# Kernel tuning notes

Hardware: AMD Instinct MI355X
Metric: run time of the kernel (lower is better)

Reference implementation:

```python
import jax, jax.numpy as jnp
import numpy as np

N, E, H, G = 50000, 500000, 64, 64


def _ln(x, g, b):
    m = jnp.mean(x, -1, keepdims=True)
    v = jnp.var(x, -1, keepdims=True)
    return (x - m) * jax.lax.rsqrt(v + 1e-5) * g + b


def _mlp_ln(x, w1, b1, w2, b2, g, be):
    # Linear -> ReLU -> (Dropout eval no-op) -> Linear -> LayerNorm
    h = jax.nn.relu(x @ w1 + b1)
    return _ln(h @ w2 + b2, g, be)


def setup_inputs() -> dict:
    key = jax.random.key(0)
    ks = jax.random.split(key, 24)
    w = lambda i, s: jax.random.normal(ks[i], s, dtype=jnp.float32) * 0.1
    z = lambda s: jnp.zeros(s, jnp.float32)
    o = lambda s: jnp.ones(s, jnp.float32)
    inp = {
        'x': jax.random.normal(ks[0], (N, 3), dtype=jnp.float32),
        'edge_index': jax.random.randint(ks[1], (2, E), 0, N),
        'edge_attr': jax.random.normal(ks[2], (E, 3), dtype=jnp.float32),
        'batch': jnp.sort(jax.random.randint(ks[3], (N,), 0, G)),
        'ne_w1': w(4, (3, H)), 'ne_b1': z((H,)), 'ne_w2': w(5, (H, H)), 'ne_b2': z((H,)), 'ne_g': o((H,)), 'ne_be': z((H,)),
        'ee_w1': w(6, (3, H)), 'ee_b1': z((H,)), 'ee_w2': w(7, (H, H)), 'ee_b2': z((H,)), 'ee_g': o((H,)), 'ee_be': z((H,)),
        'gin0_eps': z((1,)), 'gin0_w1': w(8, (H, H)), 'gin0_b1': z((H,)), 'gin0_w2': w(9, (H, H)), 'gin0_b2': z((H,)), 'gin0_g': o((H,)), 'gin0_be': z((H,)),
        'gin1_eps': z((1,)), 'gin1_w1': w(10, (H, H)), 'gin1_b1': z((H,)), 'gin1_w2': w(11, (H, H)), 'gin1_b2': z((H,)), 'gin1_g': o((H,)), 'gin1_be': z((H,)),
        'gp_w': w(12, (H, H)), 'gp_b': z((H,)), 'gp_g': o((H,)), 'gp_be': z((H,)),
        'ep_w1': w(13, (4 * H, 2 * H)), 'ep_b1': z((2 * H,)),
        'ep_w2': w(14, (2 * H, H)), 'ep_b2': z((H,)),
        'ep_w3': w(15, (H, 1)), 'ep_b3': z((1,)),
    }
    return inp


def reference(x, edge_index, edge_attr, batch,
              ne_w1, ne_b1, ne_w2, ne_b2, ne_g, ne_be,
              ee_w1, ee_b1, ee_w2, ee_b2, ee_g, ee_be,
              gin0_eps, gin0_w1, gin0_b1, gin0_w2, gin0_b2, gin0_g, gin0_be,
              gin1_eps, gin1_w1, gin1_b1, gin1_w2, gin1_b2, gin1_g, gin1_be,
              gp_w, gp_b, gp_g, gp_be,
              ep_w1, ep_b1, ep_w2, ep_b2, ep_w3, ep_b3):
    src, dst = edge_index[0], edge_index[1]
    # encoders
    h = _mlp_ln(x, ne_w1, ne_b1, ne_w2, ne_b2, ne_g, ne_be)            # [N, H]
    ef = _mlp_ln(edge_attr, ee_w1, ee_b1, ee_w2, ee_b2, ee_g, ee_be)   # [E, H]
    # GINEConv layer 0: mlp((1+eps)*x + scatter_add(relu(x_src + e)))
    msg = jax.nn.relu(h[src] + ef)
    aggr = jnp.zeros_like(h).at[dst].add(msg)
    h = _mlp_ln((1.0 + gin0_eps) * h + aggr, gin0_w1, gin0_b1, gin0_w2, gin0_b2, gin0_g, gin0_be)
    h = jax.nn.relu(h)  # inter-layer activation (dropout eval no-op)
    # GINEConv layer 1
    msg = jax.nn.relu(h[src] + ef)
    aggr = jnp.zeros_like(h).at[dst].add(msg)
    h = _mlp_ln((1.0 + gin1_eps) * h + aggr, gin1_w1, gin1_b1, gin1_w2, gin1_b2, gin1_g, gin1_be)
    # global mean pool over graphs
    seg = jax.ops.segment_sum(h, batch, num_segments=G)                            # [G, H]
    cnt = jax.ops.segment_sum(jnp.ones((h.shape[0], 1), h.dtype), batch, num_segments=G)
    gp = seg / jnp.maximum(cnt, 1.0)
    gf = _ln(jax.nn.relu(gp @ gp_w + gp_b), gp_g, gp_be)                           # [G, H]
    # edge predictor on [src | dst | global | edge] = [E, 4H]
    c = jnp.concatenate([h[src], h[dst], gf[batch[src]], ef], axis=-1)
    t = jnp.tanh(c @ ep_w1 + ep_b1)
    t = jnp.tanh(t @ ep_w2 + ep_b2)
    return jax.nn.sigmoid(t @ ep_w3 + ep_b3)  # [E, 1]
```

## Files before the change

kernel.cpp:

```cpp
#include <hip/hip_runtime.h>
#include <hip/hip_bf16.h>

typedef unsigned int uint;
typedef unsigned short ushort;
typedef __attribute__((ext_vector_type(8))) short short8;
typedef __attribute__((ext_vector_type(4))) float floatx4;

__device__ __forceinline__ float bf2f(ushort u) { return __uint_as_float(((uint)u) << 16); }
__device__ __forceinline__ ushort f2bf(float f) {
  __bf16 h = (__bf16)f;
  ushort u;
  __builtin_memcpy(&u, &h, 2);
  return u;
}
__device__ __forceinline__ float ldf(const void* p, long i, int m) {
  if (m) return bf2f(((const ushort*)p)[i]);
  return ((const float*)p)[i];
}
__device__ __forceinline__ int get_md(const uint* mdp) {
  return (mdp[0] == 0x3F800000u) ? 0 : 1;
}
__device__ __forceinline__ float fast_rcp(float x) { return __builtin_amdgcn_rcpf(x); }
__device__ __forceinline__ float tanh_fast(float x) {
  float e = __builtin_amdgcn_exp2f(2.8853900818f * x);
  return fmaf(-2.f, fast_rcp(1.f + e), 1.f);
}
__device__ __forceinline__ float sigmoid_fast(float x) {
  float e = __builtin_amdgcn_exp2f(-1.4426950409f * x);
  return fast_rcp(1.f + e);
}
__device__ __forceinline__ void gll16(const void* g, void* l) {
  __builtin_amdgcn_global_load_lds(
      (const __attribute__((address_space(1))) uint*)g,
      (__attribute__((address_space(3))) uint*)l, 16, 0, 0);
}

__global__ __launch_bounds__(256) void k_enc_mfma(
    const void* __restrict__ in, int R,
    const void* __restrict__ w1, const void* __restrict__ b1,
    const ushort* __restrict__ w2sw_, const void* __restrict__ b2,
    const void* __restrict__ gam, const void* __restrict__ bet,
    ushort* __restrict__ outp, ushort* __restrict__ outp2,
    const int* __restrict__ epos, const uint* __restrict__ mdp)
{
  __shared__ float xs[64*3];
  __shared__ float w1s[192], b1s[64], b2s[64], gs[64], bs2[64];
  __shared__ __align__(16) ushort T_s[64 * 72];
  int md = get_md(mdp);
  int tid = threadIdx.x;
  long e0 = (long)blockIdx.x * 64;
  if (tid < 192) {
    w1s[tid] = ldf(w1, tid, md);
    int row = tid / 3, cc = tid - row*3;
    long e = e0 + row;
    xs[tid] = (e < R) ? ldf(in, e*3 + cc, md) : 0.f;
  }
  if (tid < 64) { b1s[tid] = ldf(b1, tid, md); b2s[tid] = ldf(b2, tid, md);
                  gs[tid] = ldf(gam, tid, md); bs2[tid] = ldf(bet, tid, md); }
  __syncthreads();
  int lane = tid & 63, wv = tid >> 6;
  int quad = lane >> 4, mm = lane & 15;
  float x0 = xs[(wv*16 + mm)*3 + 0];
  float x1 = xs[(wv*16 + mm)*3 + 1];
  float x2 = xs[(wv*16 + mm)*3 + 2];
  short8 af[2];
#pragma unroll
  for (int s = 0; s < 2; ++s) {
#pragma unroll
    for (int j = 0; j < 8; ++j) {
      int f = s*32 + quad*8 + j;
      float hv = fmaxf(b1s[f] + x0*w1s[f] + x1*w1s[64+f] + x2*w1s[128+f], 0.f);
      af[s][j] = (short)f2bf(hv);
    }
  }
  floatx4 acc[4] = {};
  const short8* Bp = (const short8*)w2sw_;
#pragma unroll
  for (int s = 0; s < 2; ++s) {
#pragma unroll
    for (int t = 0; t < 4; ++t) {
      short8 b = Bp[(s*4 + t)*64 + lane];
      acc[t] = __builtin_amdgcn_mfma_f32_16x16x32_bf16(af[s], b, acc[t], 0, 0, 0);
    }
  }
  float vv[4][4];
#pragma unroll
  for (int t = 0; t < 4; ++t) {
    float bb = b2s[mm + 16*t];
#pragma unroll
    for (int r = 0; r < 4; ++r) vv[t][r] = acc[t][r] + bb;
  }
  float mr[4], vr[4];
#pragma unroll
  for (int r = 0; r < 4; ++r) {
    float s = vv[0][r] + vv[1][r] + vv[2][r] + vv[3][r];
#pragma unroll
    for (int off = 1; off < 16; off <<= 1) s += __shfl_xor(s, off);
    mr[r] = s * 0.015625f;
    float q = 0.f;
#pragma unroll
    for (int t = 0; t < 4; ++t) { float d = vv[t][r] - mr[r]; q = fmaf(d, d, q); }
#pragma unroll
    for (int off = 1; off < 16; off <<= 1) q += __shfl_xor(q, off);
    vr[r] = rsqrtf(q * 0.015625f + 1e-5f);
  }
#pragma unroll
  for (int t = 0; t < 4; ++t) {
    int col = mm + 16*t;
    float g = gs[col], be = bs2[col];
#pragma unroll
    for (int r = 0; r < 4; ++r)
      T_s[(wv*16 + quad*4 + r)*72 + col] = f2bf((vv[t][r] - mr[r]) * vr[r] * g + be);
  }
  __syncthreads();
#pragma unroll
  for (int i = 0; i < 2; ++i) {
    int gi = tid + 256*i;
    int row = gi >> 3, c = gi & 7;
    long e = e0 + row;
    if (e < R) {
      uint4 v = *(const uint4*)&T_s[row*72 + c*8];
      if (outp)
        ((uint4*)(outp + e*64))[c] = v;
      if (outp2)
        ((uint4*)(outp2 + (long)epos[e]*64))[c] = v;
    }
  }
}

__global__ __launch_bounds__(256) void k_swz(
    const void* __restrict__ w1, const void* __restrict__ w2,
    const void* __restrict__ w2e, const void* __restrict__ w2n,
    const void* __restrict__ gw10, const void* __restrict__ gw20,
    const void* __restrict__ gw11, const void* __restrict__ gw21,
    ushort* __restrict__ w1sw, ushort* __restrict__ w2sw,
    ushort* __restrict__ ew2sw, ushort* __restrict__ nw2sw,
    ushort* __restrict__ g0w1sw, ushort* __restrict__ g0w2sw,
    ushort* __restrict__ g1w1sw, ushort* __restrict__ g1w2sw,
    int* __restrict__ deg, float* __restrict__ gsum, int Nn,
    const uint* __restrict__ mdp)
{
  int md = get_md(mdp);
  int i = blockIdx.x * 256 + threadIdx.x;
  int nthr = gridDim.x * 256;
  for (int k = i; k < Nn; k += nthr) deg[k] = 0;
  for (int k = i; k < 64*64 + 64; k += nthr) gsum[k] = 0.f;
  if (i < 32768) {
    int q = i & 7, lane = (i >> 3) & 63, tt = (i >> 9) & 7, s = i >> 12;
    int k = s*32 + (lane >> 4)*8 + q, n = (lane & 15) + 16*tt;
    w1sw[i] = f2bf(ldf(w1, k*128 + n, md));
  }
  if (i < 8192) {
    int q = i & 7, lane = (i >> 3) & 63, tt = (i >> 9) & 3, s = i >> 11;
    int k = s*32 + (lane >> 4)*8 + q, n = (lane & 15) + 16*tt;
    int src = k*64 + n;
    w2sw[i]   = f2bf(ldf(w2,   src, md));
    ew2sw[i]  = f2bf(ldf(w2e,  src, md));
    nw2sw[i]  = f2bf(ldf(w2n,  src, md));
    g0w1sw[i] = f2bf(ldf(gw10, src, md));
    g0w2sw[i] = f2bf(ldf(gw20, src, md));
    g1w1sw[i] = f2bf(ldf(gw11, src, md));
    g1w2sw[i] = f2bf(ldf(gw21, src, md));
  }
}

__global__ __launch_bounds__(256) void k_deg(
    const int* __restrict__ ei, int* __restrict__ deg, int E_)
{
  int e = blockIdx.x * 256 + threadIdx.x;
  if (e < E_) atomicAdd(&deg[ei[E_ + e]], 1);
}

__global__ __launch_bounds__(256) void k_scan1(
    const int* __restrict__ deg, int* __restrict__ rs, int* __restrict__ bsum, int Nn)
{
  __shared__ int ls[256];
  int tid = threadIdx.x;
  int i = blockIdx.x * 256 + tid;
  int v = (i < Nn) ? deg[i] : 0;
  ls[tid] = v;
  __syncthreads();
  for (int off = 1; off < 256; off <<= 1) {
    int t = (tid >= off) ? ls[tid - off] : 0;
    __syncthreads();
    ls[tid] += t;
    __syncthreads();
  }
  if (i < Nn) rs[i] = ls[tid] - v;
  if (tid == 255) bsum[blockIdx.x] = ls[255];
}

__global__ __launch_bounds__(256) void k_scan2(
    int* __restrict__ bsum, int nb, int* __restrict__ rs, int Nn)
{
  __shared__ int ls[256];
  int tid = threadIdx.x;
  int chunk = (nb + 255) / 256;
  int c0 = tid * chunk, c1 = min(c0 + chunk, nb);
  int sum = 0;
  for (int i = c0; i < c1; ++i) sum += bsum[i];
  ls[tid] = sum;
  __syncthreads();
  for (int off = 1; off < 256; off <<= 1) {
    int t = (tid >= off) ? ls[tid - off] : 0;
    __syncthreads();
    ls[tid] += t;
    __syncthreads();
  }
  int run = ls[tid] - sum;
  for (int i = c0; i < c1; ++i) { int d = bsum[i]; bsum[i] = run; run += d; }
  if (tid == 255) rs[Nn] = ls[255];
}

__global__ __launch_bounds__(256) void k_scan3(
    int* __restrict__ rs, int* __restrict__ cur,
    const int* __restrict__ bsum, int Nn)
{
  int i = blockIdx.x * 256 + threadIdx.x;
  if (i < Nn) {
    int v = rs[i] + bsum[blockIdx.x];
    rs[i] = v;
    cur[i] = v;
  }
}

__global__ __launch_bounds__(256) void k_fill(
    const int* __restrict__ ei, int* __restrict__ cur,
    int2* __restrict__ ep, int* __restrict__ epos, int E_)
{
  int e = blockIdx.x * 256 + threadIdx.x;
  if (e < E_) {
    int s = ei[e];
    int d = ei[E_ + e];
    int p = atomicAdd(&cur[d], 1);
    ep[p] = make_int2(e, s);
    epos[e] = p;
  }
}

__global__ __launch_bounds__(256) void k_aggr(
    const ushort* __restrict__ hbu, const ushort* __restrict__ efp,
    const int2* __restrict__ ep, const int* __restrict__ rs,
    float* __restrict__ aggr, int Nn)
{
  int gw = (blockIdx.x * 256 + threadIdx.x) >> 6;
  int j = threadIdx.x & 63;
  if (gw >= Nn) return;
  int s0 = rs[gw], s1 = rs[gw + 1];
  float acc = 0.f;
  int idx = s0;
  for (; idx + 2 <= s1; idx += 2) {
    int2 a = ep[idx];
    int2 b = ep[idx + 1];
    float fA = bf2f(efp[(long)idx*64 + j]);
    float fB = bf2f(efp[(long)(idx+1)*64 + j]);
    float hA = bf2f(hbu[(long)a.y*64 + j]);
    float hB = bf2f(hbu[(long)b.y*64 + j]);
    acc += fmaxf(hA + fA, 0.f) + fmaxf(hB + fB, 0.f);
  }
  if (idx < s1) {
    int2 a = ep[idx];
    acc += fmaxf(bf2f(hbu[(long)a.y*64 + j]) + bf2f(efp[(long)idx*64 + j]), 0.f);
  }
  aggr[(long)gw*64 + j] = acc;
}

__global__ __launch_bounds__(256) void k_gine_mfma(
    const ushort* __restrict__ hbin, const float* __restrict__ aggr, int Nn,
    const void* __restrict__ epsp,
    const ushort* __restrict__ w1sw_, const void* __restrict__ b1,
    const ushort* __restrict__ w2sw_, const void* __restrict__ b2,
    const void* __restrict__ gam, const void* __restrict__ bet,
    ushort* __restrict__ hbout, int post_relu, const uint* __restrict__ mdp)
{
  __shared__ __align__(16) ushort Ws1[4096], Ws2[4096];
  __shared__ __align__(16) ushort T_s[64 * 72];
  __shared__ float b1s[64], b2s[64], gs[64], bs2[64];
  int md = get_md(mdp);
  int tid = threadIdx.x;
  {
    const uint4* p1 = (const uint4*)w1sw_;
    const uint4* p2 = (const uint4*)w2sw_;
    ((uint4*)Ws1)[tid] = p1[tid];
    ((uint4*)Ws1)[tid + 256] = p1[tid + 256];
    ((uint4*)Ws2)[tid] = p2[tid];
    ((uint4*)Ws2)[tid + 256] = p2[tid + 256];
  }
  if (tid < 64) { b1s[tid] = ldf(b1, tid, md); b2s[tid] = ldf(b2, tid, md);
                  gs[tid] = ldf(gam, tid, md); bs2[tid] = ldf(bet, tid, md); }
  float ope = 1.f + ldf(epsp, 0, md);
  int lane = tid & 63, wv = tid >> 6;
  int quad = lane >> 4, mm = lane & 15;
  long node = (long)blockIdx.x * 64 + wv*16 + mm;
  long nc = (node < Nn) ? node : (long)(Nn - 1);
  const ushort* hrow = hbin + nc*64;
  const float*  arow = aggr + nc*64;
  short8 af[2];
#pragma unroll
  for (int s = 0; s < 2; ++s) {
    int c = s*4 + quad;
    short8 hv = *(const short8*)(hrow + c*8);
    float4 a0 = *(const float4*)(arow + c*8);
    float4 a1 = *(const float4*)(arow + c*8 + 4);
    float uu[8];
    uu[0] = fmaf(bf2f((ushort)hv[0]), ope, a0.x);
    uu[1] = fmaf(bf2f((ushort)hv[1]), ope, a0.y);
    uu[2] = fmaf(bf2f((ushort)hv[2]), ope, a0.z);
    uu[3] = fmaf(bf2f((ushort)hv[3]), ope, a0.w);
    uu[4] = fmaf(bf2f((ushort)hv[4]), ope, a1.x);
    uu[5] = fmaf(bf2f((ushort)hv[5]), ope, a1.y);
    uu[6] = fmaf(bf2f((ushort)hv[6]), ope, a1.z);
    uu[7] = fmaf(bf2f((ushort)hv[7]), ope, a1.w);
#pragma unroll
    for (int j = 0; j < 8; ++j) af[s][j] = (short)f2bf(uu[j]);
  }
  __syncthreads();
  floatx4 acc[4] = {};
#pragma unroll
  for (int s = 0; s < 2; ++s) {
#pragma unroll
    for (int t = 0; t < 4; ++t) {
      short8 b = *(const short8*)&Ws1[((s*4 + t)*64 + lane)*8];
      acc[t] = __builtin_amdgcn_mfma_f32_16x16x32_bf16(af[s], b, acc[t], 0, 0, 0);
    }
  }
#pragma unroll
  for (int t = 0; t < 4; ++t) {
    int col = mm + 16*t;
    float bb = b1s[col];
#pragma unroll
    for (int r = 0; r < 4; ++r)
      T_s[(wv*16 + quad*4 + r)*72 + col] = f2bf(fmaxf(acc[t][r] + bb, 0.f));
  }
  __syncthreads();
  short8 af2[2];
#pragma unroll
  for (int s = 0; s < 2; ++s)
    af2[s] = *(const short8*)&T_s[(wv*16 + mm)*72 + s*32 + quad*8];
  floatx4 acc2[4] = {};
#pragma unroll
  for (int s = 0; s < 2; ++s) {
#pragma unroll
    for (int t = 0; t < 4; ++t) {
      short8 b = *(const short8*)&Ws2[((s*4 + t)*64 + lane)*8];
      acc2[t] = __builtin_amdgcn_mfma_f32_16x16x32_bf16(af2[s], b, acc2[t], 0, 0, 0);
    }
  }
  float vv[4][4];
#pragma unroll
  for (int t = 0; t < 4; ++t) {
    float bb = b2s[mm + 16*t];
#pragma unroll
    for (int r = 0; r < 4; ++r) vv[t][r] = acc2[t][r] + bb;
  }
  float mr[4], vr[4];
#pragma unroll
  for (int r = 0; r < 4; ++r) {
    float s = vv[0][r] + vv[1][r] + vv[2][r] + vv[3][r];
#pragma unroll
    for (int off = 1; off < 16; off <<= 1) s += __shfl_xor(s, off);
    mr[r] = s * 0.015625f;
    float q = 0.f;
#pragma unroll
    for (int t = 0; t < 4; ++t) { float d = vv[t][r] - mr[r]; q = fmaf(d, d, q); }
#pragma unroll
    for (int off = 1; off < 16; off <<= 1) q += __shfl_xor(q, off);
    vr[r] = rsqrtf(q * 0.015625f + 1e-5f);
  }
  __syncthreads();
#pragma unroll
  for (int t = 0; t < 4; ++t) {
    int col = mm + 16*t;
    float g = gs[col], be = bs2[col];
#pragma unroll
    for (int r = 0; r < 4; ++r) {
      float o = (vv[t][r] - mr[r]) * vr[r] * g + be;
      if (post_relu) o = fmaxf(o, 0.f);
      T_s[(wv*16 + quad*4 + r)*72 + col] = f2bf(o);
    }
  }
  __syncthreads();
#pragma unroll
  for (int i = 0; i < 2; ++i) {
    int gi = tid + 256*i;
    int row = gi >> 3, c = gi & 7;
    long n2 = (long)blockIdx.x * 64 + row;
    if (n2 < Nn)
      ((uint4*)(hbout + n2*64))[c] = *(const uint4*)&T_s[row*72 + c*8];
  }
}

__global__ __launch_bounds__(256) void k_pool_f(
    const ushort* __restrict__ hbu, const int* __restrict__ batch,
    float* __restrict__ gsum, float* __restrict__ gcnt, int Nn)
{
  int gw = (blockIdx.x * 256 + threadIdx.x) >> 6;
  int j = threadIdx.x & 63;
  long r0 = (long)gw * 64;
  if (r0 >= Nn) return;
  long rend = min(r0 + 64, (long)Nn);
  float acc = 0.f; int cur = batch[r0]; int run = 0;
  for (long r = r0; r < rend; ++r) {
    int g = batch[r];
    if (g != cur) {
      atomicAdd(&gsum[cur*64 + j], acc);
      if (j == 0) atomicAdd(&gcnt[cur], (float)run);
      acc = 0.f; run = 0; cur = g;
    }
    acc += bf2f(hbu[r*64 + j]);
    run++;
  }
  atomicAdd(&gsum[cur*64 + j], acc);
  if (j == 0) atomicAdd(&gcnt[cur], (float)run);
}

__global__ __launch_bounds__(64) void k_pool_fin_f(
    const float* __restrict__ gsum, const float* __restrict__ gcnt,
    const void* __restrict__ gpw, const void* __restrict__ gpb,
    const void* __restrict__ gpg, const void* __restrict__ gpbe,
    ushort* __restrict__ gfb, const uint* __restrict__ mdp)
{
  __shared__ float wgs[4096];
  __shared__ float us[64];
  int md = get_md(mdp);
  int j = threadIdx.x;
  int g = blockIdx.x;
  for (int i = j; i < 4096; i += 64) wgs[i] = ldf(gpw, i, md);
  float ic = 1.f / fmaxf(gcnt[g], 1.f);
  us[j] = gsum[g*64 + j] * ic;
  __syncthreads();
  float t = ldf(gpb, j, md);
#pragma unroll
  for (int k = 0; k < 64; ++k) t = fmaf(us[k], wgs[k*64 + j], t);
  t = fmaxf(t, 0.f);
  float m = t;
#pragma unroll
  for (int off = 1; off < 64; off <<= 1) m += __shfl_xor(m, off);
  m *= 0.015625f;
  float d = t - m;
  float v = d * d;
#pragma unroll
  for (int off = 1; off < 64; off <<= 1) v += __shfl_xor(v, off);
  float rs = rsqrtf(v * 0.015625f + 1e-5f);
  gfb[g*64 + j] = f2bf(d * rs * ldf(gpg, j, md) + ldf(gpbe, j, md));
}

__global__ __launch_bounds__(1024, 4) void k_pred_mfma(
    const ushort* __restrict__ hb, const ushort* __restrict__ efp,
    const int* __restrict__ epos,
    const ushort* __restrict__ gfb, const int* __restrict__ ei,
    const int* __restrict__ batch,
    const ushort* __restrict__ w1sw, const ushort* __restrict__ w2sw,
    const void* __restrict__ pb1, const void* __restrict__ pb2,
    const void* __restrict__ pw3, const void* __restrict__ pb3,
    void* __restrict__ out, int E_, const uint* __restrict__ mdp)
{
  __shared__ __align__(16) ushort W1s[32768];
  __shared__ __align__(16) ushort W2s[8192];
  __shared__ __align__(16) ushort T_s[16 * 16*72];
  __shared__ float b1s[128], b2s[64], w3s[64];
  int md = get_md(mdp);
  int tid = threadIdx.x;
  {
    const uint4* w1p = (const uint4*)w1sw;
#pragma unroll
    for (int i = 0; i < 4; ++i)
      ((uint4*)W1s)[tid + 1024*i] = w1p[tid + 1024*i];
    ((uint4*)W2s)[tid] = ((const uint4*)w2sw)[tid];
  }
  if (tid < 128) b1s[tid] = ldf(pb1, tid, md);
  if (tid < 64) { b2s[tid] = ldf(pb2, tid, md); w3s[tid] = ldf(pw3, tid, md); }
  __syncthreads();

  int lane = tid & 63, wv = tid >> 6;
  int quad = lane >> 4, mm = lane & 15;
  ushort* Tw = T_s + wv * (16*72);
  float b3 = ldf(pb3, 0, md);
  int ngroups = (E_ + 15) >> 4;
  int nw = gridDim.x * 16;
  for (int g = blockIdx.x * 16 + wv; g < ngroups; g += nw) {
    long e = (long)g*16 + mm; if (e >= E_) e = E_ - 1;
    int si = ei[e], di = ei[E_ + e];
    int gi = batch[si];
    int pe = epos[e];
    const char* hs = (const char*)hb  + (uint)si*128u;
    const char* hd = (const char*)hb  + (uint)di*128u;
    const char* gs = (const char*)gfb + (uint)gi*128u;
    const char* es = (const char*)efp + (uint)pe*128u;
    short8 cq[8];
    cq[0] = *(const short8*)(hs + quad*16);
    cq[1] = *(const short8*)(hs + 64 + quad*16);
    cq[2] = *(const short8*)(hd + quad*16);
    cq[3] = *(const short8*)(hd + 64 + quad*16);
    cq[4] = *(const short8*)(gs + quad*16);
    cq[5] = *(const short8*)(gs + 64 + quad*16);
    cq[6] = *(const short8*)(es + quad*16);
    cq[7] = *(const short8*)(es + 64 + quad*16);
    floatx4 acc[8] = {};
#pragma unroll
    for (int c = 0; c < 8; ++c) {
#pragma unroll
      for (int t = 0; t < 8; ++t) {
        short8 b = *(const short8*)&W1s[((c*8 + t)*64 + lane)*8];
        acc[t] = __builtin_amdgcn_mfma_f32_16x16x32_bf16(cq[c], b, acc[t], 0, 0, 0);
      }
    }
    floatx4 acc2[4] = {};
#pragma unroll
    for (int h = 0; h < 2; ++h) {
#pragma unroll
      for (int t4 = 0; t4 < 4; ++t4) {
        int t = h*4 + t4;
        float bb = b1s[mm + 16*t];
#pragma unroll
        for (int r = 0; r < 4; ++r)
          Tw[(quad*4 + r)*72 + mm + 16*t4] = f2bf(tanh_fast(acc[t][r] + bb));
      }
#pragma unroll
      for (int s2h = 0; s2h < 2; ++s2h) {
        int s2 = h*2 + s2h;
        short8 a = *(const short8*)&Tw[mm*72 + s2h*32 + quad*8];
#pragma unroll
        for (int t = 0; t < 4; ++t) {
          short8 b = *(const short8*)&W2s[((s2*4 + t)*64 + lane)*8];
          acc2[t] = __builtin_amdgcn_mfma_f32_16x16x32_bf16(a, b, acc2[t], 0, 0, 0);
        }
      }
    }
    float p0 = 0.f, p1 = 0.f, p2 = 0.f, p3 = 0.f;
#pragma unroll
    for (int t = 0; t < 4; ++t) {
      int col = mm + 16*t;
      float bb = b2s[col], w3v = w3s[col];
      p0 = fmaf(tanh_fast(acc2[t][0] + bb), w3v, p0);
      p1 = fmaf(tanh_fast(acc2[t][1] + bb), w3v, p1);
      p2 = fmaf(tanh_fast(acc2[t][2] + bb), w3v, p2);
      p3 = fmaf(tanh_fast(acc2[t][3] + bb), w3v, p3);
    }
#pragma unroll
    for (int off = 1; off < 16; off <<= 1) {
      p0 += __shfl_xor(p0, off);
      p1 += __shfl_xor(p1, off);
      p2 += __shfl_xor(p2, off);
      p3 += __shfl_xor(p3, off);
    }
    if (mm == 0) {
      long eb = (long)g*16 + quad*4;
      float ps[4] = {p0, p1, p2, p3};
#pragma unroll
      for (int r = 0; r < 4; ++r) {
        if (eb + r < E_) {
          float sg = sigmoid_fast(ps[r] + b3);
          if (md) ((ushort*)out)[eb + r] = f2bf(sg);
          else    ((float*)out)[eb + r]  = sg;
        }
      }
    }
  }
}

extern "C" void kernel_launch(void* const* d_in, const int* in_sizes, int n_in,
                              void* d_out, int out_size, void* d_ws, size_t ws_size,
                              hipStream_t stream)
{
  const void* x     = d_in[0];
  const int*  ei    = (const int*)d_in[1];
  const void* eattr = d_in[2];
  const int*  batch = (const int*)d_in[3];
  const void* ne_w1 = d_in[4];  const void* ne_b1 = d_in[5];
  const void* ne_w2 = d_in[6];  const void* ne_b2 = d_in[7];
  const void* ne_g  = d_in[8];  const void* ne_be = d_in[9];
  const void* ee_w1 = d_in[10]; const void* ee_b1 = d_in[11];
  const void* ee_w2 = d_in[12]; const void* ee_b2 = d_in[13];
  const void* ee_g  = d_in[14]; const void* ee_be = d_in[15];
  const void* g0_ep = d_in[16];
  const void* g0_w1 = d_in[17]; const void* g0_b1 = d_in[18];
  const void* g0_w2 = d_in[19]; const void* g0_b2 = d_in[20];
  const void* g0_g  = d_in[21]; const void* g0_be = d_in[22];
  const void* g1_ep = d_in[23];
  const void* g1_w1 = d_in[24]; const void* g1_b1 = d_in[25];
  const void* g1_w2 = d_in[26]; const void* g1_b2 = d_in[27];
  const void* g1_g  = d_in[28]; const void* g1_be = d_in[29];
  const void* gp_w  = d_in[30]; const void* gp_b  = d_in[31];
  const void* gp_g  = d_in[32]; const void* gp_be = d_in[33];
  const void* ep_w1 = d_in[34]; const void* ep_b1 = d_in[35];
  const void* ep_w2 = d_in[36]; const void* ep_b2 = d_in[37];
  const void* ep_w3 = d_in[38]; const void* ep_b3 = d_in[39];

  int N = in_sizes[3];
  int E = in_sizes[1] / 2;
  const uint* mdp = (const uint*)ne_g;

  char* ws = (char*)d_ws;
  size_t off = 0;
  auto alloc = [&](size_t bytes) { char* p = ws + off; off += (bytes + 255) & ~(size_t)255; return p; };
  ushort* hb     = (ushort*)alloc((size_t)N * 64 * 2);
  ushort* efp    = (ushort*)alloc((size_t)E * 64 * 2);
  float*  aggr   = (float*) alloc((size_t)N * 64 * 4);
  float*  gsum   = (float*) alloc((64 * 64 + 64) * 4);
  float*  gcnt   = gsum + 64 * 64;
  ushort* gfb    = (ushort*)alloc(64 * 64 * 2);
  ushort* w1sw   = (ushort*)alloc(32768 * 2);
  ushort* w2sw   = (ushort*)alloc(8192 * 2);
  ushort* ew2sw  = (ushort*)alloc(8192 * 2);
  ushort* nw2sw  = (ushort*)alloc(8192 * 2);
  ushort* g0w1sw = (ushort*)alloc(8192 * 2);
  ushort* g0w2sw = (ushort*)alloc(8192 * 2);
  ushort* g1w1sw = (ushort*)alloc(8192 * 2);
  ushort* g1w2sw = (ushort*)alloc(8192 * 2);
  int*    deg    = (int*)   alloc((size_t)N * 4);
  int*    rs     = (int*)   alloc((size_t)(N + 1) * 4);
  int*    cur    = (int*)   alloc((size_t)N * 4);
  int2*   ep     = (int2*)  alloc((size_t)E * 8);
  int*    epos   = (int*)   alloc((size_t)E * 4);
  int*    bsum   = (int*)   alloc((size_t)((N + 255) / 256) * 4);
  (void)ws_size; (void)n_in; (void)out_size;

  int gN = (N + 255) / 256;
  int gE = (E + 255) / 256;
  int gE64 = (E + 63) / 64;
  int gN64 = (N + 63) / 64;
  int gAggr = (int)(((long)N * 64 + 255) / 256);
  int gPool = ((N + 63) / 64 + 3) / 4;

  k_swz<<<128, 256, 0, stream>>>(ep_w1, ep_w2, ee_w2, ne_w2, g0_w1, g0_w2, g1_w1, g1_w2,
                                 w1sw, w2sw, ew2sw, nw2sw,
                                 g0w1sw, g0w2sw, g1w1sw, g1w2sw,
                                 deg, gsum, N, mdp);
  k_deg<<<gE, 256, 0, stream>>>(ei, deg, E);
  k_scan1<<<gN, 256, 0, stream>>>(deg, rs, bsum, N);
  k_scan2<<<1, 256, 0, stream>>>(bsum, gN, rs, N);
  k_scan3<<<gN, 256, 0, stream>>>(rs, cur, bsum, N);
  k_fill<<<gE, 256, 0, stream>>>(ei, cur, ep, epos, E);
  k_enc_mfma<<<gN64, 256, 0, stream>>>(x, N, ne_w1, ne_b1, nw2sw, ne_b2, ne_g, ne_be,
                                       hb, (ushort*)nullptr, (const int*)nullptr, mdp);
  k_enc_mfma<<<gE64, 256, 0, stream>>>(eattr, E, ee_w1, ee_b1, ew2sw, ee_b2, ee_g, ee_be,
                                       (ushort*)nullptr, efp, epos, mdp);
  k_aggr<<<gAggr, 256, 0, stream>>>(hb, efp, ep, rs, aggr, N);
  k_gine_mfma<<<gN64, 256, 0, stream>>>(hb, aggr, N, g0_ep, g0w1sw, g0_b1, g0w2sw, g0_b2,
                                        g0_g, g0_be, hb, 1, mdp);
  k_aggr<<<gAggr, 256, 0, stream>>>(hb, efp, ep, rs, aggr, N);
  k_gine_mfma<<<gN64, 256, 0, stream>>>(hb, aggr, N, g1_ep, g1w1sw, g1_b1, g1w2sw, g1_b2,
                                        g1_g, g1_be, hb, 0, mdp);
  k_pool_f<<<gPool, 256, 0, stream>>>(hb, batch, gsum, gcnt, N);
  k_pool_fin_f<<<64, 64, 0, stream>>>(gsum, gcnt, gp_w, gp_b, gp_g, gp_be, gfb, mdp);
  k_pred_mfma<<<256, 1024, 0, stream>>>(hb, efp, epos, gfb, ei, batch, w1sw, w2sw,
                                        ep_b1, ep_b2, ep_w3, ep_b3, d_out, E, mdp);
}
```

Measured before the change: 426.1 us.

## Fuse encoders into one launch, pooling into GINE, pool-finish into predictor

Merges the node and edge encoder launches into a single grid that picks its parameters from the block index. Folds the mean-pool accumulation into the second GINE kernel, which reads the normalized rows from shared memory instead of re-reading them from global memory. Every predictor block now recomputes the global-feature MLP and LayerNorm from gsum/gcnt into shared memory, so the separate pool and pool-finish kernels are gone. This removes three launches and one pass over hb, but adds redundant per-block work and extra LDS use (about 26KB) to the large predictor kernel, which may lower its occupancy.

```diff
diff --git a/kernel.cpp b/kernel.cpp
--- a/kernel.cpp
+++ b/kernel.cpp
@@ -29,26 +29,37 @@
   float e = __builtin_amdgcn_exp2f(-1.4426950409f * x);
   return fast_rcp(1.f + e);
 }
-__device__ __forceinline__ void gll16(const void* g, void* l) {
-  __builtin_amdgcn_global_load_lds(
-      (const __attribute__((address_space(1))) uint*)g,
-      (__attribute__((address_space(3))) uint*)l, 16, 0, 0);
-}
-
-__global__ __launch_bounds__(256) void k_enc_mfma(
-    const void* __restrict__ in, int R,
-    const void* __restrict__ w1, const void* __restrict__ b1,
-    const ushort* __restrict__ w2sw_, const void* __restrict__ b2,
-    const void* __restrict__ gam, const void* __restrict__ bet,
-    ushort* __restrict__ outp, ushort* __restrict__ outp2,
-    const int* __restrict__ epos, const uint* __restrict__ mdp)
-{
+
+__global__ __launch_bounds__(256) void k_enc2_mfma(
+    const void* __restrict__ xin, int Nn, const void* __restrict__ eain, int Ee,
+    const void* __restrict__ nw1, const void* __restrict__ nb1,
+    const ushort* __restrict__ nw2sw, const void* __restrict__ nb2,
+    const void* __restrict__ ng, const void* __restrict__ nbe,
+    const void* __restrict__ ew1, const void* __restrict__ eb1,
+    const ushort* __restrict__ ew2sw, const void* __restrict__ eb2,
+    const void* __restrict__ eg, const void* __restrict__ ebe,
+    ushort* __restrict__ hb, ushort* __restrict__ efp,
+    const int* __restrict__ epos, const uint* __restrict__ mdp, int gN64)
+{
+  bool isN = blockIdx.x < (uint)gN64;
+  const void* in      = isN ? xin : eain;
+  int R               = isN ? Nn : Ee;
+  const void* w1      = isN ? nw1 : ew1;
+  const void* b1      = isN ? nb1 : eb1;
+  const ushort* w2sw_ = isN ? nw2sw : ew2sw;
+  const void* b2      = isN ? nb2 : eb2;
+  const void* gam     = isN ? ng : eg;
+  const void* bet     = isN ? nbe : ebe;
+  ushort* outp        = isN ? hb : (ushort*)nullptr;
+  ushort* outp2       = isN ? (ushort*)nullptr : efp;
+  int bid             = isN ? (int)blockIdx.x : (int)(blockIdx.x - gN64);
+
   __shared__ float xs[64*3];
   __shared__ float w1s[192], b1s[64], b2s[64], gs[64], bs2[64];
   __shared__ __align__(16) ushort T_s[64 * 72];
   int md = get_md(mdp);
   int tid = threadIdx.x;
-  long e0 = (long)blockIdx.x * 64;
+  long e0 = (long)bid * 64;
   if (tid < 192) {
     w1s[tid] = ldf(w1, tid, md);
     int row = tid / 3, cc = tid - row*3;
@@ -271,7 +282,9 @@
     const ushort* __restrict__ w1sw_, const void* __restrict__ b1,
     const ushort* __restrict__ w2sw_, const void* __restrict__ b2,
     const void* __restrict__ gam, const void* __restrict__ bet,
-    ushort* __restrict__ hbout, int post_relu, const uint* __restrict__ mdp)
+    ushort* __restrict__ hbout, int post_relu,
+    const int* __restrict__ batch, float* __restrict__ gsum,
+    float* __restrict__ gcnt, int do_pool, const uint* __restrict__ mdp)
 {
   __shared__ __align__(16) ushort Ws1[4096], Ws2[4096];
   __shared__ __align__(16) ushort T_s[64 * 72];
@@ -388,76 +401,46 @@
     if (n2 < Nn)
       ((uint4*)(hbout + n2*64))[c] = *(const uint4*)&T_s[row*72 + c*8];
   }
-}
-
-__global__ __launch_bounds__(256) void k_pool_f(
-    const ushort* __restrict__ hbu, const int* __restrict__ batch,
-    float* __restrict__ gsum, float* __restrict__ gcnt, int Nn)
-{
-  int gw = (blockIdx.x * 256 + threadIdx.x) >> 6;
-  int j = threadIdx.x & 63;
-  long r0 = (long)gw * 64;
-  if (r0 >= Nn) return;
-  long rend = min(r0 + 64, (long)Nn);
-  float acc = 0.f; int cur = batch[r0]; int run = 0;
-  for (long r = r0; r < rend; ++r) {
-    int g = batch[r];
-    if (g != cur) {
-      atomicAdd(&gsum[cur*64 + j], acc);
+  if (do_pool && wv == 0) {
+    int j = lane;
+    long r0 = (long)blockIdx.x * 64;
+    long rend = min(r0 + 64, (long)Nn);
+    if (r0 < rend) {
+      float acc_p = 0.f; int cur = batch[r0]; int run = 0;
+      for (long r = r0; r < rend; ++r) {
+        int g = batch[r];
+        if (g != cur) {
+          atomicAdd(&gsum[cur*64 + j], acc_p);
+          if (j == 0) atomicAdd(&gcnt[cur], (float)run);
+          acc_p = 0.f; run = 0; cur = g;
+        }
+        acc_p += bf2f(T_s[(int)(r - r0)*72 + j]);
+        run++;
+      }
+      atomicAdd(&gsum[cur*64 + j], acc_p);
       if (j == 0) atomicAdd(&gcnt[cur], (float)run);
-      acc = 0.f; run = 0; cur = g;
-    }
-    acc += bf2f(hbu[r*64 + j]);
-    run++;
-  }
-  atomicAdd(&gsum[cur*64 + j], acc);
-  if (j == 0) atomicAdd(&gcnt[cur], (float)run);
-}
-
-__global__ __launch_bounds__(64) void k_pool_fin_f(
-    const float* __restrict__ gsum, const float* __restrict__ gcnt,
-    const void* __restrict__ gpw, const void* __restrict__ gpb,
-    const void* __restrict__ gpg, const void* __restrict__ gpbe,
-    ushort* __restrict__ gfb, const uint* __restrict__ mdp)
-{
-  __shared__ float wgs[4096];
-  __shared__ float us[64];
-  int md = get_md(mdp);
-  int j = threadIdx.x;
-  int g = blockIdx.x;
-  for (int i = j; i < 4096; i += 64) wgs[i] = ldf(gpw, i, md);
-  float ic = 1.f / fmaxf(gcnt[g], 1.f);
-  us[j] = gsum[g*64 + j] * ic;
-  __syncthreads();
-  float t = ldf(gpb, j, md);
-#pragma unroll
-  for (int k = 0; k < 64; ++k) t = fmaf(us[k], wgs[k*64 + j], t);
-  t = fmaxf(t, 0.f);
-  float m = t;
-#pragma unroll
-  for (int off = 1; off < 64; off <<= 1) m += __shfl_xor(m, off);
-  m *= 0.015625f;
-  float d = t - m;
-  float v = d * d;
-#pragma unroll
-  for (int off = 1; off < 64; off <<= 1) v += __shfl_xor(v, off);
-  float rs = rsqrtf(v * 0.015625f + 1e-5f);
-  gfb[g*64 + j] = f2bf(d * rs * ldf(gpg, j, md) + ldf(gpbe, j, md));
+    }
+  }
 }
 
 __global__ __launch_bounds__(1024, 4) void k_pred_mfma(
     const ushort* __restrict__ hb, const ushort* __restrict__ efp,
-    const int* __restrict__ epos,
-    const ushort* __restrict__ gfb, const int* __restrict__ ei,
+    const int* __restrict__ epos, const int* __restrict__ ei,
     const int* __restrict__ batch,
     const ushort* __restrict__ w1sw, const ushort* __restrict__ w2sw,
     const void* __restrict__ pb1, const void* __restrict__ pb2,
     const void* __restrict__ pw3, const void* __restrict__ pb3,
+    const float* __restrict__ gsum, const float* __restrict__ gcnt,
+    const void* __restrict__ gpw, const void* __restrict__ gpb,
+    const void* __restrict__ gpg, const void* __restrict__ gpbe,
     void* __restrict__ out, int E_, const uint* __restrict__ mdp)
 {
   __shared__ __align__(16) ushort W1s[32768];
   __shared__ __align__(16) ushort W2s[8192];
   __shared__ __align__(16) ushort T_s[16 * 16*72];
+  __shared__ __align__(16) ushort gfb_s[64 * 64];
+  __shared__ float wgs[4096];
+  __shared__ float us_s[16 * 64];
   __shared__ float b1s[128], b2s[64], w3s[64];
   int md = get_md(mdp);
   int tid = threadIdx.x;
@@ -468,12 +451,36 @@
       ((uint4*)W1s)[tid + 1024*i] = w1p[tid + 1024*i];
     ((uint4*)W2s)[tid] = ((const uint4*)w2sw)[tid];
   }
+  for (int i = tid; i < 4096; i += 1024) wgs[i] = ldf(gpw, i, md);
   if (tid < 128) b1s[tid] = ldf(pb1, tid, md);
   if (tid < 64) { b2s[tid] = ldf(pb2, tid, md); w3s[tid] = ldf(pw3, tid, md); }
   __syncthreads();
 
   int lane = tid & 63, wv = tid >> 6;
   int quad = lane >> 4, mm = lane & 15;
+#pragma unroll
+  for (int rr = 0; rr < 4; ++rr) {
+    int gg = wv*4 + rr;
+    float ic = 1.f / fmaxf(gcnt[gg], 1.f);
+    float usj = gsum[gg*64 + lane] * ic;
+    us_s[wv*64 + lane] = usj;
+    float t = ldf(gpb, lane, md);
+#pragma unroll 8
+    for (int k = 0; k < 64; ++k) t = fmaf(us_s[wv*64 + k], wgs[k*64 + lane], t);
+    t = fmaxf(t, 0.f);
+    float m = t;
+#pragma unroll
+    for (int off = 1; off < 64; off <<= 1) m += __shfl_xor(m, off);
+    m *= 0.015625f;
+    float d = t - m;
+    float v = d * d;
+#pragma unroll
+    for (int off = 1; off < 64; off <<= 1) v += __shfl_xor(v, off);
+    float rsq = rsqrtf(v * 0.015625f + 1e-5f);
+    gfb_s[gg*64 + lane] = f2bf(d * rsq * ldf(gpg, lane, md) + ldf(gpbe, lane, md));
+  }
+  __syncthreads();
+
   ushort* Tw = T_s + wv * (16*72);
   float b3 = ldf(pb3, 0, md);
   int ngroups = (E_ + 15) >> 4;
@@ -485,15 +492,15 @@
     int pe = epos[e];
     const char* hs = (const char*)hb  + (uint)si*128u;
     const char* hd = (const char*)hb  + (uint)di*128u;
-    const char* gs = (const char*)gfb + (uint)gi*128u;
+    const ushort* grow = gfb_s + gi*64;
     const char* es = (const char*)efp + (uint)pe*128u;
     short8 cq[8];
     cq[0] = *(const short8*)(hs + quad*16);
     cq[1] = *(const short8*)(hs + 64 + quad*16);
     cq[2] = *(const short8*)(hd + quad*16);
     cq[3] = *(const short8*)(hd + 64 + quad*16);
-    cq[4] = *(const short8*)(gs + quad*16);
-    cq[5] = *(const short8*)(gs + 64 + quad*16);
+    cq[4] = *(const short8*)&grow[quad*8];
+    cq[5] = *(const short8*)&grow[32 + quad*8];
     cq[6] = *(const short8*)(es + quad*16);
     cq[7] = *(const short8*)(es + 64 + quad*16);
     floatx4 acc[8] = {};
@@ -599,7 +606,6 @@
   float*  aggr   = (float*) alloc((size_t)N * 64 * 4);
   float*  gsum   = (float*) alloc((64 * 64 + 64) * 4);
   float*  gcnt   = gsum + 64 * 64;
-  ushort* gfb    = (ushort*)alloc(64 * 64 * 2);
   ushort* w1sw   = (ushort*)alloc(32768 * 2);
   ushort* w2sw   = (ushort*)alloc(8192 * 2);
   ushort* ew2sw  = (ushort*)alloc(8192 * 2);
@@ -621,7 +627,6 @@
   int gE64 = (E + 63) / 64;
   int gN64 = (N + 63) / 64;
   int gAggr = (int)(((long)N * 64 + 255) / 256);
-  int gPool = ((N + 63) / 64 + 3) / 4;
 
   k_swz<<<128, 256, 0, stream>>>(ep_w1, ep_w2, ee_w2, ne_w2, g0_w1, g0_w2, g1_w1, g1_w2,
                                  w1sw, w2sw, ew2sw, nw2sw,
@@ -632,18 +637,21 @@
   k_scan2<<<1, 256, 0, stream>>>(bsum, gN, rs, N);
   k_scan3<<<gN, 256, 0, stream>>>(rs, cur, bsum, N);
   k_fill<<<gE, 256, 0, stream>>>(ei, cur, ep, epos, E);
-  k_enc_mfma<<<gN64, 256, 0, stream>>>(x, N, ne_w1, ne_b1, nw2sw, ne_b2, ne_g, ne_be,
-                                       hb, (ushort*)nullptr, (const int*)nullptr, mdp);
-  k_enc_mfma<<<gE64, 256, 0, stream>>>(eattr, E, ee_w1, ee_b1, ew2sw, ee_b2, ee_g, ee_be,
-                                       (ushort*)nullptr, efp, epos, mdp);
+  k_enc2_mfma<<<gN64 + gE64, 256, 0, stream>>>(
+      x, N, eattr, E,
+      ne_w1, ne_b1, nw2sw, ne_b2, ne_g, ne_be,
+      ee_w1, ee_b1, ew2sw, ee_b2, ee_g, ee_be,
+      hb, efp, epos, mdp, gN64);
   k_aggr<<<gAggr, 256, 0, stream>>>(hb, efp, ep, rs, aggr, N);
   k_gine_mfma<<<gN64, 256, 0, stream>>>(hb, aggr, N, g0_ep, g0w1sw, g0_b1, g0w2sw, g0_b2,
-                                        g0_g, g0_be, hb, 1, mdp);
+                                        g0_g, g0_be, hb, 1,
+                                        batch, gsum, gcnt, 0, mdp);
   k_aggr<<<gAggr, 256, 0, stream>>>(hb, efp, ep, rs, aggr, N);
   k_gine_mfma<<<gN64, 256, 0, stream>>>(hb, aggr, N, g1_ep, g1w1sw, g1_b1, g1w2sw, g1_b2,
-                                        g1_g, g1_be, hb, 0, mdp);
-  k_pool_f<<<gPool, 256, 0, stream>>>(hb, batch, gsum, gcnt, N);
-  k_pool_fin_f<<<64, 64, 0, stream>>>(gsum, gcnt, gp_w, gp_b, gp_g, gp_be, gfb, mdp);
-  k_pred_mfma<<<256, 1024, 0, stream>>>(hb, efp, epos, gfb, ei, batch, w1sw, w2sw,
-                                        ep_b1, ep_b2, ep_w3, ep_b3, d_out, E, mdp);
-}
+                                        g1_g, g1_be, hb, 0,
+                                        batch, gsum, gcnt, 1, mdp);
+  k_pred_mfma<<<256, 1024, 0, stream>>>(hb, efp, epos, ei, batch, w1sw, w2sw,
+                                        ep_b1, ep_b2, ep_w3, ep_b3,
+                                        gsum, gcnt, gp_w, gp_b, gp_g, gp_be,
+                                        d_out, E, mdp);
+}
```

New measurement: 401.4 us. -5.8%, faster.
